# Optimization experiments

Measured on AMD Instinct MI355X. Metric: run time of the kernel, lower is better.

## Reference

```python
import jax, jax.numpy as jnp
import numpy as np

EPS = 1e-5
GROUPS = 8

def group_norm(x, gamma, beta):
    # x: [B,C,H,W], 8 groups
    B, C, H, W = x.shape
    xg = x.reshape(B, GROUPS, C // GROUPS, H, W)
    mu = jnp.mean(xg, axis=(2, 3, 4), keepdims=True)
    var = jnp.mean((xg - mu) ** 2, axis=(2, 3, 4), keepdims=True)
    xn = ((xg - mu) * jax.lax.rsqrt(var + EPS)).reshape(B, C, H, W)
    return xn * gamma[None, :, None, None] + beta[None, :, None, None]

def setup_inputs() -> dict:
    key = jax.random.key(0)
    ks = jax.random.split(key, 7)
    B, C, H, W = 4, 256, 64, 64
    x = jax.random.normal(ks[0], (B, C, H, W), dtype=jnp.float32)
    gamma = jnp.ones((C,), dtype=jnp.float32)
    beta = jnp.zeros((C,), dtype=jnp.float32)
    s = 1.0 / np.sqrt(C)
    w_qkv = jax.random.normal(ks[1], (3 * C, C), dtype=jnp.float32) * s
    b_qkv = jnp.zeros((3 * C,), dtype=jnp.float32)
    w_proj = jax.random.normal(ks[2], (C, C), dtype=jnp.float32) * s
    b_proj = jnp.zeros((C,), dtype=jnp.float32)
    return {"x": x, "gamma": gamma, "beta": beta, "w_qkv": w_qkv,
            "b_qkv": b_qkv, "w_proj": w_proj, "b_proj": b_proj}

def reference(x, gamma, beta, w_qkv, b_qkv, w_proj, b_proj):
    B, C, H, W = x.shape
    N = H * W
    h = group_norm(x, gamma, beta)
    # 1x1 conv == per-pixel matmul
    qkv = jnp.einsum('bchw,oc->bohw', h, w_qkv) + b_qkv[None, :, None, None]
    q, k, v = jnp.split(qkv, 3, axis=1)  # each [B,C,H,W]
    q = q.reshape(B, C, N).transpose(0, 2, 1)   # [B,N,C]
    k = k.reshape(B, C, N)                      # [B,C,N]
    v = v.reshape(B, C, N).transpose(0, 2, 1)   # [B,N,C]
    attn = jax.nn.softmax(jnp.einsum('bnc,bcm->bnm', q, k) / jnp.sqrt(jnp.float32(C)), axis=-1)
    out = jnp.einsum('bnm,bmc->bnc', attn, v)   # [B,N,C]
    out = out.transpose(0, 2, 1).reshape(B, C, H, W)
    proj = jnp.einsum('bchw,oc->bohw', out, w_proj) + b_proj[None, :, None, None]
    return x + proj
```

## Files before the change

### kernel.cpp

```cpp
#include <hip/hip_runtime.h>
#include <hip/hip_bf16.h>
#include <math.h>

#define B 4
#define C 256
#define G 8
#define N 4096
#define EPSV 1e-5f
#define SCALE 0.0625f

typedef __attribute__((ext_vector_type(8))) short short8;
typedef __attribute__((ext_vector_type(16))) float f32x16;
typedef unsigned short ushort_t;
typedef unsigned int uint_t;

__device__ __forceinline__ ushort_t f2bf(float f) {
    union { float f; uint_t u; } c; c.f = f;
    uint_t u = c.u;
    uint_t r = (u + 0x7FFFu + ((u >> 16) & 1u)) >> 16;
    return (ushort_t)r;
}
__device__ __forceinline__ float bf2f(ushort_t h) {
    union { uint_t u; float f; } c; c.u = ((uint_t)h) << 16;
    return c.f;
}
__device__ __forceinline__ uint_t pack2(float a, float b) {
    return (uint_t)f2bf(a) | ((uint_t)f2bf(b) << 16);
}
__device__ __forceinline__ uint_t cvtpk_bf16(float lo, float hi) {
    uint_t r;
    asm("v_cvt_pk_bf16_f32 %0, %1, %2" : "=v"(r) : "v"(lo), "v"(hi));
    return r;
}
__device__ __forceinline__ void gl_lds16(const void* g, void* l) {
    __builtin_amdgcn_global_load_lds(
        (const __attribute__((address_space(1))) void*)g,
        (__attribute__((address_space(3))) void*)l, 16, 0, 0);
}

__global__ __launch_bounds__(256) void wconv(const float* __restrict__ wq,
        const float* __restrict__ wp, ushort_t* __restrict__ wbf) {
    int idx = blockIdx.x*256 + threadIdx.x;
    #pragma unroll
    for (int p = 0; p < 4; p++) {
        int id = idx + p*16384;
        float4 v = (id < 49152) ? ((const float4*)wq)[id] : ((const float4*)wp)[id - 49152];
        uint2 pk; pk.x = pack2(v.x, v.y); pk.y = pack2(v.z, v.w);
        *(uint2*)&wbf[(size_t)id*4] = pk;
    }
}

__global__ __launch_bounds__(256) void gn_partial(const float* __restrict__ x,
                                                  float* __restrict__ partials) {
    int blk = blockIdx.x;
    int bg = blk >> 3;
    int part = blk & 7;
    const float4* xp4 = (const float4*)(x + (size_t)bg * (32 * N) + (size_t)part * (32 * N / 8));
    float s = 0.f, ss = 0.f;
    for (int i = threadIdx.x; i < 4096; i += 256) {
        float4 v = xp4[i];
        s  += v.x + v.y + v.z + v.w;
        ss += v.x*v.x + v.y*v.y + v.z*v.z + v.w*v.w;
    }
    __shared__ float rs[256], rss[256];
    rs[threadIdx.x] = s; rss[threadIdx.x] = ss;
    __syncthreads();
    for (int off = 128; off > 0; off >>= 1) {
        if (threadIdx.x < off) {
            rs[threadIdx.x]  += rs[threadIdx.x + off];
            rss[threadIdx.x] += rss[threadIdx.x + off];
        }
        __syncthreads();
    }
    if (threadIdx.x == 0) {
        partials[(bg*8 + part)*2]     = rs[0];
        partials[(bg*8 + part)*2 + 1] = rss[0];
    }
}

__global__ void gn_final(const float* __restrict__ partials, float* __restrict__ stats) {
    int t = threadIdx.x;
    if (t < 32) {
        float s = 0.f, ss = 0.f;
        for (int p = 0; p < 8; p++) {
            s  += partials[(t*8 + p)*2];
            ss += partials[(t*8 + p)*2 + 1];
        }
        const float inv = 1.f / 131072.f;
        float mu = s * inv;
        float var = fmaxf(ss * inv - mu*mu, 0.f);
        stats[t*2]     = mu;
        stats[t*2 + 1] = rsqrtf(var + EPSV);
    }
}

__global__ __launch_bounds__(256) void norm_bf16(const float* __restrict__ x,
        const float* __restrict__ gamma, const float* __restrict__ beta,
        const float* __restrict__ stats, ushort_t* __restrict__ hbf) {
    int b = blockIdx.z, c0 = blockIdx.y*64, n0 = blockIdx.x*64;
    int t = threadIdx.x;
    int cq = t >> 4, nq = t & 15;
    ushort_t hv[4][4];
    #pragma unroll
    for (int i = 0; i < 4; i++) {
        int c = c0 + cq*4 + i;
        int g = c >> 5;
        float mu = stats[(b*G+g)*2], rs = stats[(b*G+g)*2+1];
        float ga = gamma[c]*rs;
        float be = beta[c] - mu*ga;
        float4 v = *(const float4*)&x[((size_t)(b*C + c))*N + n0 + nq*4];
        hv[i][0] = f2bf(v.x*ga + be);
        hv[i][1] = f2bf(v.y*ga + be);
        hv[i][2] = f2bf(v.z*ga + be);
        hv[i][3] = f2bf(v.w*ga + be);
    }
    #pragma unroll
    for (int j = 0; j < 4; j++) {
        uint2 pk;
        pk.x = (uint_t)hv[0][j] | ((uint_t)hv[1][j]<<16);
        pk.y = (uint_t)hv[2][j] | ((uint_t)hv[3][j]<<16);
        *(uint2*)&hbf[((size_t)(b*N + n0 + nq*4 + j))*256 + c0 + cq*4] = pk;
    }
}

__global__ __launch_bounds__(256) void qkv_mfma(const ushort_t* __restrict__ hbf,
        const ushort_t* __restrict__ wbf, const float* __restrict__ bias,
        ushort_t* __restrict__ qbf, ushort_t* __restrict__ kimg, ushort_t* __restrict__ vimg) {
    int b = blockIdx.z, o0 = blockIdx.y*128, n0 = blockIdx.x*128;
    int tid = threadIdx.x;
    int w = tid>>6, l = tid&63, l31 = l&31, lh = l>>5;
    __shared__ short Ws[2][8192];
    __shared__ short Hs[2][8192];

    const ushort_t* wb = wbf + (size_t)o0*256;
    const ushort_t* hb = hbf + ((size_t)b*N + n0)*256;

    auto stage = [&](int bb, int c0) {
        #pragma unroll
        for (int q = 0; q < 4; q++) {
            int u0 = (q*4 + w)*64;
            int u  = u0 + l;
            int row = u & 127, ch = u >> 7;
            gl_lds16(wb + (size_t)row*256 + c0 + ch*8, &Ws[bb][u0*8]);
            gl_lds16(hb + (size_t)row*256 + c0 + ch*8, &Hs[bb][u0*8]);
        }
    };

    f32x16 acc[4];
    #pragma unroll
    for (int nf = 0; nf < 4; nf++)
        #pragma unroll
        for (int r = 0; r < 16; r++) acc[nf][r] = 0.f;

    stage(0, 0);
    __syncthreads();
    for (int t = 0; t < 4; t++) {
        int bb = t & 1;
        if (t < 3) stage(bb^1, (t+1)*64);
        short8 af[4];
        #pragma unroll
        for (int s = 0; s < 4; s++)
            af[s] = *(const short8*)&Ws[bb][((2*s+lh)*128 + w*32 + l31)*8];
        #pragma unroll
        for (int nf = 0; nf < 4; nf++) {
            #pragma unroll
            for (int s = 0; s < 4; s++) {
                short8 hf = *(const short8*)&Hs[bb][((2*s+lh)*128 + nf*32 + l31)*8];
                acc[nf] = __builtin_amdgcn_mfma_f32_32x32x16_bf16(af[s], hf, acc[nf], 0, 0, 0);
            }
        }
        __syncthreads();
    }

    int ow = o0 + w*32;
    float bv[16];
    #pragma unroll
    for (int r = 0; r < 16; r++) bv[r] = bias[ow + (r&3) + 8*(r>>2) + 4*lh];

    if (ow < 256) {
        #pragma unroll
        for (int nf = 0; nf < 4; nf++) {
            int n = n0 + nf*32 + l31;
            ushort_t* row = qbf + ((size_t)(b*N + n))*256 + ow;
            #pragma unroll
            for (int rp = 0; rp < 8; rp++) {
                int r0 = rp*2;
                int cl = (r0&3) + 8*(r0>>2) + 4*lh;
                uint_t wd = cvtpk_bf16((acc[nf][r0]+bv[r0])*SCALE, (acc[nf][r0+1]+bv[r0+1])*SCALE);
                *(uint_t*)(row + cl) = wd;
            }
        }
    } else if (ow < 512) {
        int cb = ow - 256;
        #pragma unroll
        for (int nf = 0; nf < 4; nf++) {
            int n = n0 + nf*32 + l31;
            ushort_t* tbase = kimg + (size_t)b*1048576 + (size_t)(n>>5)*8192
                            + (size_t)l31*8 + 4*lh;
            #pragma unroll
            for (int g = 0; g < 4; g++) {
                uint2 pk;
                pk.x = pack2(acc[nf][g*4+0]+bv[g*4+0], acc[nf][g*4+1]+bv[g*4+1]);
                pk.y = pack2(acc[nf][g*4+2]+bv[g*4+2], acc[nf][g*4+3]+bv[g*4+3]);
                *(uint2*)(tbase + (size_t)((cb>>3)+g)*256) = pk;
            }
        }
    } else {
        int cb = ow - 512;
        #pragma unroll
        for (int nf = 0; nf < 4; nf++) {
            int n = n0 + nf*32 + l31;
            ushort_t* tbase = vimg + (size_t)b*1048576 + (size_t)(n>>5)*8192
                            + (size_t)(l31>>3)*2048 + (l31&7);
            #pragma unroll
            for (int r = 0; r < 16; r++) {
                int cl = (r&3) + 8*(r>>2) + 4*lh;
                tbase[(size_t)(cb+cl)*8] = f2bf(acc[nf][r] + bv[r]);
            }
        }
    }
}

__global__ __launch_bounds__(256, 1) void attn_mfma(const ushort_t* __restrict__ qbf,
        const ushort_t* __restrict__ kimg, const ushort_t* __restrict__ vimg,
        ushort_t* __restrict__ part, float* __restrict__ ml) {
    int f = blockIdx.x;
    int qt  = f >> 3;
    int b   = (f >> 1) & 3;
    int kvh = f & 1;
    constexpr int NT = 64;
    int w = threadIdx.x >> 6;
    int l = threadIdx.x & 63;
    int l31 = l & 31, lh = l >> 5;

    __shared__ short KV[3][2][8192];

    int qbase = qt*128 + w*32;
    short8 qf[16];
    {
        const ushort_t* qrow = qbf + ((size_t)(b*N + qbase + l31))*256;
        #pragma unroll
        for (int s = 0; s < 16; s++)
            qf[s] = *(const short8*)(qrow + s*16 + lh*8);
    }

    f32x16 ot[8];
    #pragma unroll
    for (int mc = 0; mc < 8; mc++)
        #pragma unroll
        for (int r = 0; r < 16; r++) ot[mc][r] = 0.f;
    float m = -INFINITY, lsum = 0.f;

    const char* kbase = (const char*)kimg + (size_t)b*2097152;
    const char* vbase = (const char*)vimg + (size_t)b*2097152;
    int m0base = kvh*2048;

    auto stage = [&](int slot, int t) {
        int tile = (m0base >> 5) + t;
        const char* kt = kbase + (size_t)tile*16384;
        const char* vt = vbase + (size_t)tile*16384;
        #pragma unroll
        for (int q = 0; q < 4; q++) {
            int u0 = (w*4 + q)*64;
            gl_lds16(kt + (u0 + l)*16, &KV[slot][0][u0*8]);
            gl_lds16(vt + (u0 + l)*16, &KV[slot][1][u0*8]);
        }
    };

    auto qk_issue = [&](int slot, f32x16& s0, f32x16& s1) {
        #pragma unroll
        for (int r = 0; r < 16; r++) { s0[r] = 0.f; s1[r] = 0.f; }
        const short* kb_ = &KV[slot][0][0];
        #pragma unroll
        for (int s = 0; s < 8; s++) {
            short8 ka = *(const short8*)(kb_ + ((size_t)((4*s   + lh)*32 + l31))*8);
            short8 kc = *(const short8*)(kb_ + ((size_t)((4*s+2 + lh)*32 + l31))*8);
            s0 = __builtin_amdgcn_mfma_f32_32x32x16_bf16(ka, qf[2*s],   s0, 0, 0, 0);
            s1 = __builtin_amdgcn_mfma_f32_32x32x16_bf16(kc, qf[2*s+1], s1, 0, 0, 0);
        }
    };

    auto body = [&](int t, f32x16& sc0, f32x16& sc1, f32x16& sn0, f32x16& sn1) {
        __syncthreads();
        int slot0 = t % 3;
        int slot1 = (t+1) % 3;
        int slot2 = (t+2) % 3;
        if (t+1 < NT) qk_issue(slot1, sn0, sn1);
        if (t+2 < NT) stage(slot2, t+2);

        float sv[16];
        #pragma unroll
        for (int r = 0; r < 16; r++) sv[r] = sc0[r] + sc1[r];
        float pmax = sv[0];
        #pragma unroll
        for (int r = 1; r < 16; r++) pmax = fmaxf(pmax, sv[r]);
        pmax = fmaxf(pmax, __shfl_xor(pmax, 32));
        if (!__all(pmax <= m + 8.0f)) {
            float mn = fmaxf(m, pmax);
            float fac = __expf(m - mn);
            m = mn;
            lsum *= fac;
            #pragma unroll
            for (int mc = 0; mc < 8; mc++)
                #pragma unroll
                for (int r = 0; r < 16; r++) ot[mc][r] *= fac;
        }
        float p[16]; float ls = 0.f;
        #pragma unroll
        for (int r = 0; r < 16; r++) { p[r] = __expf(sv[r] - m); ls += p[r]; }
        ls += __shfl_xor(ls, 32);
        lsum += ls;

        short8 pf0, pf1;
        {
            uint_t x0 = cvtpk_bf16(p[0], p[1]);
            uint_t y0 = cvtpk_bf16(p[4], p[5]);
            uint_t x1 = cvtpk_bf16(p[2], p[3]);
            uint_t y1 = cvtpk_bf16(p[6], p[7]);
            auto r0 = __builtin_amdgcn_permlane32_swap(x0, y0, false, false);
            auto r1 = __builtin_amdgcn_permlane32_swap(x1, y1, false, false);
            union { uint_t u[4]; short8 s8; } u_;
            u_.u[0] = r0[0]; u_.u[1] = r1[0]; u_.u[2] = r0[1]; u_.u[3] = r1[1];
            pf0 = u_.s8;
            uint_t x2 = cvtpk_bf16(p[8],  p[9]);
            uint_t y2 = cvtpk_bf16(p[12], p[13]);
            uint_t x3 = cvtpk_bf16(p[10], p[11]);
            uint_t y3 = cvtpk_bf16(p[14], p[15]);
            auto r2 = __builtin_amdgcn_permlane32_swap(x2, y2, false, false);
            auto r3 = __builtin_amdgcn_permlane32_swap(x3, y3, false, false);
            union { uint_t u[4]; short8 s8; } u2_;
            u2_.u[0] = r2[0]; u2_.u[1] = r3[0]; u2_.u[2] = r2[1]; u2_.u[3] = r3[1];
            pf1 = u2_.s8;
        }

        const short* vb_ = &KV[slot0][1][0];
        #pragma unroll
        for (int mc = 0; mc < 8; mc++) {
            short8 v0 = *(const short8*)(vb_ + ((size_t)((lh)*256   + mc*32 + l31))*8);
            short8 v1 = *(const short8*)(vb_ + ((size_t)((2+lh)*256 + mc*32 + l31))*8);
            ot[mc] = __builtin_amdgcn_mfma_f32_32x32x16_bf16(v0, pf0, ot[mc], 0, 0, 0);
            ot[mc] = __builtin_amdgcn_mfma_f32_32x32x16_bf16(v1, pf1, ot[mc], 0, 0, 0);
        }
    };

    f32x16 stA0, stA1, stB0, stB1;

    stage(0, 0);
    __syncthreads();
    qk_issue(0, stA0, stA1);
    stage(1, 1);

    for (int t = 0; t < NT; t += 2) {
        body(t,   stA0, stA1, stB0, stB1);
        body(t+1, stB0, stB1, stA0, stA1);
    }

    float invl = 1.f / lsum;
    ushort_t* pbase = part + (size_t)kvh*4194304 + ((size_t)(b*N + qbase + l31))*256;
    #pragma unroll
    for (int mc = 0; mc < 8; mc++)
        #pragma unroll
        for (int rp = 0; rp < 8; rp++) {
            int r0 = rp*2;
            uint_t wd = cvtpk_bf16(ot[mc][r0]*invl, ot[mc][r0+1]*invl);
            int c0 = (r0 & 3) + 8*(r0 >> 2) + 4*lh + 32*mc;
            *(uint_t*)(pbase + c0) = wd;
        }
    if (l < 32) {
        size_t row = (size_t)kvh*16384 + b*4096 + qbase + l;
        ml[row*2]     = m;
        ml[row*2 + 1] = lsum;
    }
}

__global__ __launch_bounds__(256) void attn_merge(const ushort_t* __restrict__ part,
        const float* __restrict__ ml, ushort_t* __restrict__ ob) {
    int t = blockIdx.x*256 + threadIdx.x;
    int row = t >> 5;
    int c8 = (t & 31) * 8;
    float m0 = ml[(size_t)row*2],           l0 = ml[(size_t)row*2 + 1];
    float m1 = ml[(size_t)(16384 + row)*2], l1 = ml[(size_t)(16384 + row)*2 + 1];
    float M = fmaxf(m0, m1);
    float w0 = __expf(m0 - M) * l0, w1 = __expf(m1 - M) * l1;
    float inv = 1.f / (w0 + w1);
    w0 *= inv; w1 *= inv;
    const ushort_t* p0 = part + (size_t)row*256 + c8;
    const ushort_t* p1 = p0 + 4194304;
    float o[8];
    #pragma unroll
    for (int e = 0; e < 8; e++) o[e] = w0*bf2f(p0[e]) + w1*bf2f(p1[e]);
    uint4 pk;
    pk.x = pack2(o[0], o[1]);
    pk.y = pack2(o[2], o[3]);
    pk.z = pack2(o[4], o[5]);
    pk.w = pack2(o[6], o[7]);
    *(uint4*)(ob + (size_t)row*256 + c8) = pk;
}

__global__ __launch_bounds__(256) void proj_mfma(const ushort_t* __restrict__ obf,
        const ushort_t* __restrict__ wpbf, const float* __restrict__ bp,
        const float* __restrict__ x, float* __restrict__ out) {
    int b = blockIdx.z, o0 = blockIdx.y*128, n0 = blockIdx.x*128;
    int tid = threadIdx.x;
    int w = tid>>6, l = tid&63, l31 = l&31, lh = l>>5;
    __shared__ short Ws[2][8192];
    __shared__ short Hs[2][8192];

    const ushort_t* wb = wpbf + (size_t)o0*256;
    const ushort_t* hb = obf + ((size_t)b*N + n0)*256;

    auto stage = [&](int bb, int c0) {
        #pragma unroll
        for (int q = 0; q < 4; q++) {
            int u0 = (q*4 + w)*64;
            int u  = u0 + l;
            int row = u & 127, ch = u >> 7;
            gl_lds16(wb + (size_t)row*256 + c0 + ch*8, &Ws[bb][u0*8]);
            gl_lds16(hb + (size_t)row*256 + c0 + ch*8, &Hs[bb][u0*8]);
        }
    };

    f32x16 acc[4];
    #pragma unroll
    for (int nf = 0; nf < 4; nf++)
        #pragma unroll
        for (int r = 0; r < 16; r++) acc[nf][r] = 0.f;

    stage(0, 0);
    __syncthreads();
    for (int t = 0; t < 4; t++) {
        int bb = t & 1;
        if (t < 3) stage(bb^1, (t+1)*64);
        short8 af[4];
        #pragma unroll
        for (int s = 0; s < 4; s++)
            af[s] = *(const short8*)&Ws[bb][((2*s+lh)*128 + w*32 + l31)*8];
        #pragma unroll
        for (int nf = 0; nf < 4; nf++) {
            #pragma unroll
            for (int s = 0; s < 4; s++) {
                short8 hf = *(const short8*)&Hs[bb][((2*s+lh)*128 + nf*32 + l31)*8];
                acc[nf] = __builtin_amdgcn_mfma_f32_32x32x16_bf16(af[s], hf, acc[nf], 0, 0, 0);
            }
        }
        __syncthreads();
    }

    int cw = o0 + w*32;
    float bv[16];
    #pragma unroll
    for (int r = 0; r < 16; r++) bv[r] = bp[cw + (r&3) + 8*(r>>2) + 4*lh];

    #pragma unroll
    for (int nf = 0; nf < 4; nf++) {
        int n = n0 + nf*32 + l31;
        #pragma unroll
        for (int r = 0; r < 16; r++) {
            int cl = (r&3) + 8*(r>>2) + 4*lh;
            size_t a = ((size_t)b*C + cw + cl)*N + n;
            out[a] = acc[nf][r] + bv[r] + x[a];
        }
    }
}

extern "C" void kernel_launch(void* const* d_in, const int* in_sizes, int n_in,
                              void* d_out, int out_size, void* d_ws, size_t ws_size,
                              hipStream_t stream) {
    const float* x      = (const float*)d_in[0];
    const float* gamma  = (const float*)d_in[1];
    const float* beta   = (const float*)d_in[2];
    const float* w_qkv  = (const float*)d_in[3];
    const float* b_qkv  = (const float*)d_in[4];
    const float* w_proj = (const float*)d_in[5];
    const float* b_proj = (const float*)d_in[6];
    float* out = (float*)d_out;
    char* wsb  = (char*)d_ws;

    const size_t MB = 1048576;
    ushort_t* qbf  = (ushort_t*)(wsb);
    ushort_t* kimg = (ushort_t*)(wsb + 8*MB);
    ushort_t* vimg = (ushort_t*)(wsb + 16*MB);
    ushort_t* part = (ushort_t*)(wsb + 24*MB);
    ushort_t* hbf  = part;
    float*    ml   = (float*)  (wsb + 40*MB);
    ushort_t* ob   = (ushort_t*)(wsb + 40*MB + 524288);
    float* partials = (float*) (wsb + 48*MB + 524288);
    float* stats    = partials + 512;
    ushort_t* wbf  = (ushort_t*)(wsb + 48*MB + 524288 + 4096);

    wconv<<<dim3(64), dim3(256), 0, stream>>>(w_qkv, w_proj, wbf);
    gn_partial<<<dim3(256), dim3(256), 0, stream>>>(x, partials);
    gn_final<<<dim3(1), dim3(64), 0, stream>>>(partials, stats);
    norm_bf16<<<dim3(64, 4, 4), dim3(256), 0, stream>>>(x, gamma, beta, stats, hbf);
    qkv_mfma<<<dim3(32, 6, 4), dim3(256), 0, stream>>>(hbf, wbf, b_qkv, qbf, kimg, vimg);
    attn_mfma<<<dim3(256), dim3(256), 0, stream>>>(qbf, kimg, vimg, part, ml);
    attn_merge<<<dim3(2048), dim3(256), 0, stream>>>(part, ml, ob);
    proj_mfma<<<dim3(32, 2, 4), dim3(256), 0, stream>>>(ob, wbf + 196608, b_proj, x, out);
}
```

Baseline: 163.7 us.

## Split attention output channels across wave pairs and double the block count

```diff
diff --git a/kernel.cpp b/kernel.cpp
--- a/kernel.cpp
+++ b/kernel.cpp
@@ -221,7 +221,7 @@
     }
 }
 
-__global__ __launch_bounds__(256, 1) void attn_mfma(const ushort_t* __restrict__ qbf,
+__global__ __launch_bounds__(256, 2) void attn_mfma(const ushort_t* __restrict__ qbf,
         const ushort_t* __restrict__ kimg, const ushort_t* __restrict__ vimg,
         ushort_t* __restrict__ part, float* __restrict__ ml) {
     int f = blockIdx.x;
@@ -232,10 +232,12 @@
     int w = threadIdx.x >> 6;
     int l = threadIdx.x & 63;
     int l31 = l & 31, lh = l >> 5;
-
-    __shared__ short KV[3][2][8192];
-
-    int qbase = qt*128 + w*32;
+    int qsub = w >> 1;
+    int chv  = w & 1;
+
+    __shared__ short KV[2][2][8192];
+
+    int qbase = qt*64 + qsub*32;
     short8 qf[16];
     {
         const ushort_t* qrow = qbf + ((size_t)(b*N + qbase + l31))*256;
@@ -244,19 +246,18 @@
             qf[s] = *(const short8*)(qrow + s*16 + lh*8);
     }
 
-    f32x16 ot[8];
-    #pragma unroll
-    for (int mc = 0; mc < 8; mc++)
+    f32x16 ot[4];
+    #pragma unroll
+    for (int mc = 0; mc < 4; mc++)
         #pragma unroll
         for (int r = 0; r < 16; r++) ot[mc][r] = 0.f;
     float m = -INFINITY, lsum = 0.f;
 
     const char* kbase = (const char*)kimg + (size_t)b*2097152;
     const char* vbase = (const char*)vimg + (size_t)b*2097152;
-    int m0base = kvh*2048;
 
     auto stage = [&](int slot, int t) {
-        int tile = (m0base >> 5) + t;
+        int tile = kvh*64 + t;
         const char* kt = kbase + (size_t)tile*16384;
         const char* vt = vbase + (size_t)tile*16384;
         #pragma unroll
@@ -267,30 +268,30 @@
         }
     };
 
-    auto qk_issue = [&](int slot, f32x16& s0, f32x16& s1) {
-        #pragma unroll
-        for (int r = 0; r < 16; r++) { s0[r] = 0.f; s1[r] = 0.f; }
+    stage(0, 0);
+
+    for (int t = 0; t < NT; t++) {
+        int slot = t & 1;
+        __syncthreads();
+        if (t+1 < NT) stage(slot^1, t+1);
+
+        f32x16 st0, st1;
+        #pragma unroll
+        for (int r = 0; r < 16; r++) { st0[r] = 0.f; st1[r] = 0.f; }
         const short* kb_ = &KV[slot][0][0];
+        __builtin_amdgcn_s_setprio(1);
         #pragma unroll
         for (int s = 0; s < 8; s++) {
             short8 ka = *(const short8*)(kb_ + ((size_t)((4*s   + lh)*32 + l31))*8);
             short8 kc = *(const short8*)(kb_ + ((size_t)((4*s+2 + lh)*32 + l31))*8);
-            s0 = __builtin_amdgcn_mfma_f32_32x32x16_bf16(ka, qf[2*s],   s0, 0, 0, 0);
-            s1 = __builtin_amdgcn_mfma_f32_32x32x16_bf16(kc, qf[2*s+1], s1, 0, 0, 0);
-        }
-    };
-
-    auto body = [&](int t, f32x16& sc0, f32x16& sc1, f32x16& sn0, f32x16& sn1) {
-        __syncthreads();
-        int slot0 = t % 3;
-        int slot1 = (t+1) % 3;
-        int slot2 = (t+2) % 3;
-        if (t+1 < NT) qk_issue(slot1, sn0, sn1);
-        if (t+2 < NT) stage(slot2, t+2);
+            st0 = __builtin_amdgcn_mfma_f32_32x32x16_bf16(ka, qf[2*s],   st0, 0, 0, 0);
+            st1 = __builtin_amdgcn_mfma_f32_32x32x16_bf16(kc, qf[2*s+1], st1, 0, 0, 0);
+        }
+        __builtin_amdgcn_s_setprio(0);
 
         float sv[16];
         #pragma unroll
-        for (int r = 0; r < 16; r++) sv[r] = sc0[r] + sc1[r];
+        for (int r = 0; r < 16; r++) sv[r] = st0[r] + st1[r];
         float pmax = sv[0];
         #pragma unroll
         for (int r = 1; r < 16; r++) pmax = fmaxf(pmax, sv[r]);
@@ -301,7 +302,7 @@
             m = mn;
             lsum *= fac;
             #pragma unroll
-            for (int mc = 0; mc < 8; mc++)
+            for (int mc = 0; mc < 4; mc++)
                 #pragma unroll
                 for (int r = 0; r < 16; r++) ot[mc][r] *= fac;
         }
@@ -333,32 +334,23 @@
             pf1 = u2_.s8;
         }
 
-        const short* vb_ = &KV[slot0][1][0];
-        #pragma unroll
-        for (int mc = 0; mc < 8; mc++) {
-            short8 v0 = *(const short8*)(vb_ + ((size_t)((lh)*256   + mc*32 + l31))*8);
-            short8 v1 = *(const short8*)(vb_ + ((size_t)((2+lh)*256 + mc*32 + l31))*8);
+        const short* vb_ = &KV[slot][1][0];
+        __builtin_amdgcn_s_setprio(1);
+        #pragma unroll
+        for (int mc = 0; mc < 4; mc++) {
+            int cc = chv*4 + mc;
+            short8 v0 = *(const short8*)(vb_ + ((size_t)((lh)*256   + cc*32 + l31))*8);
+            short8 v1 = *(const short8*)(vb_ + ((size_t)((2+lh)*256 + cc*32 + l31))*8);
             ot[mc] = __builtin_amdgcn_mfma_f32_32x32x16_bf16(v0, pf0, ot[mc], 0, 0, 0);
             ot[mc] = __builtin_amdgcn_mfma_f32_32x32x16_bf16(v1, pf1, ot[mc], 0, 0, 0);
         }
-    };
-
-    f32x16 stA0, stA1, stB0, stB1;
-
-    stage(0, 0);
-    __syncthreads();
-    qk_issue(0, stA0, stA1);
-    stage(1, 1);
-
-    for (int t = 0; t < NT; t += 2) {
-        body(t,   stA0, stA1, stB0, stB1);
-        body(t+1, stB0, stB1, stA0, stA1);
+        __builtin_amdgcn_s_setprio(0);
     }
 
     float invl = 1.f / lsum;
-    ushort_t* pbase = part + (size_t)kvh*4194304 + ((size_t)(b*N + qbase + l31))*256;
-    #pragma unroll
-    for (int mc = 0; mc < 8; mc++)
+    ushort_t* pbase = part + (size_t)kvh*4194304 + ((size_t)(b*N + qbase + l31))*256 + chv*128;
+    #pragma unroll
+    for (int mc = 0; mc < 4; mc++)
         #pragma unroll
         for (int rp = 0; rp < 8; rp++) {
             int r0 = rp*2;
@@ -366,7 +358,7 @@
             int c0 = (r0 & 3) + 8*(r0 >> 2) + 4*lh + 32*mc;
             *(uint_t*)(pbase + c0) = wd;
         }
-    if (l < 32) {
+    if (chv == 0 && l < 32) {
         size_t row = (size_t)kvh*16384 + b*4096 + qbase + l;
         ml[row*2]     = m;
         ml[row*2 + 1] = lsum;
@@ -493,7 +485,7 @@
     gn_final<<<dim3(1), dim3(64), 0, stream>>>(partials, stats);
     norm_bf16<<<dim3(64, 4, 4), dim3(256), 0, stream>>>(x, gamma, beta, stats, hbf);
     qkv_mfma<<<dim3(32, 6, 4), dim3(256), 0, stream>>>(hbf, wbf, b_qkv, qbf, kimg, vimg);
-    attn_mfma<<<dim3(256), dim3(256), 0, stream>>>(qbf, kimg, vimg, part, ml);
+    attn_mfma<<<dim3(512), dim3(256), 0, stream>>>(qbf, kimg, vimg, part, ml);
     attn_merge<<<dim3(2048), dim3(256), 0, stream>>>(part, ml, ob);
     proj_mfma<<<dim3(32, 2, 4), dim3(256), 0, stream>>>(ob, wbf + 196608, b_proj, x, out);
 }
```

Measured after the change: 184.4 us. 1.13x slower.
